# Optimization experiments

Hardware: AMD Instinct MI355X
Metric: run time of the kernel (lower is better)

The kernel has to match this reference:

```python
import jax, jax.numpy as jnp
import numpy as np


def setup_inputs() -> dict:
    key = jax.random.key(0)
    k1, k2, k3, k4, k5 = jax.random.split(key, 5)
    C, H, W, hi, wi = 32, 32, 32, 32, 32
    return {
        "lx_in": jax.random.normal(k1, (C, H, W, hi, wi), dtype=jnp.float32),
        "ux_in": jax.random.normal(k2, (C, H, W, hi, wi), dtype=jnp.float32),
        "lc_in": jax.random.normal(k3, (C, H, W), dtype=jnp.float32),
        "uc_in": jax.random.normal(k4, (C, H, W), dtype=jnp.float32),
        "x_min": jax.random.uniform(k5, (hi, wi), dtype=jnp.float32),
        "x_max": jnp.ones((hi, wi), dtype=jnp.float32),
    }


def reference(lx_in, ux_in, lc_in, uc_in, x_min, x_max):
    # lx_in/ux_in: [C,H,W,hi,wi] linear coeffs over input pixels; lc_in/uc_in: [C,H,W]
    minm = x_min[None, None, None, :, :]  # broadcast of x_min.repeat(C,H,W,1,1)
    maxm = x_max[None, None, None, :, :]
    zero = jnp.zeros((), lx_in.dtype)
    # lower concrete bound: positive coeff -> x_min, negative -> x_max (sign==0 -> 0 mask)
    mask_lower = jnp.where(lx_in > 0, minm, jnp.where(lx_in < 0, maxm, zero))
    l = jnp.sum(mask_lower * lx_in, axis=(-2, -1)) + lc_in  # [C,H,W]
    # upper concrete bound: positive coeff -> x_max, negative -> x_min
    mask_upper = jnp.where(ux_in > 0, maxm, jnp.where(ux_in < 0, minm, zero))
    u = jnp.sum(mask_upper * ux_in, axis=(-2, -1)) + uc_in  # [C,H,W]

    alive = l >= 0                      # pass-through branch (applied after dead branch in torch)
    cross = (l < 0) & (u > 0)           # crossing ReLU branch
    denom = jnp.where(cross, u - l, jnp.ones((), l.dtype))  # safe division
    slope = jnp.clip(jnp.where(cross, u / denom, jnp.ones((), l.dtype)), 0.0, 1.0)

    a5 = alive[..., None, None]
    c5 = cross[..., None, None]
    s5 = slope[..., None, None]
    lx_out = jnp.where(a5, lx_in, zero)
    ux_out = jnp.where(a5, ux_in, jnp.where(c5, s5 * ux_in, zero))
    lc_out = jnp.where(alive, lc_in, zero)
    uc_out = jnp.where(alive, uc_in, jnp.where(cross, slope * uc_in - slope * l, zero))
    return (lx_out, ux_out, lc_out, uc_out)
```

## Files before the change

### kernel.cpp

```cpp
#include <hip/hip_runtime.h>

constexpr int NPIX  = 32 * 32 * 32;
constexpr int TILE  = 32 * 32;
constexpr int NBIG  = NPIX * TILE;
constexpr int THREADS = 256;

__global__ __launch_bounds__(THREADS)
void relu_conv_kernel(const float* __restrict__ lx_in,
                      const float* __restrict__ ux_in,
                      const float* __restrict__ lc_in,
                      const float* __restrict__ uc_in,
                      const float* __restrict__ x_min,
                      const float* __restrict__ x_max,
                      float* __restrict__ lx_out,
                      float* __restrict__ ux_out,
                      float* __restrict__ lc_out,
                      float* __restrict__ uc_out)
{
    const int p = blockIdx.x;
    const int t = threadIdx.x;
    const long base = (long)p * TILE + t * 4;

    const float4 lx = *(const float4*)(lx_in + base);
    const float4 ux = *(const float4*)(ux_in + base);
    const float4 mn = *(const float4*)(x_min + t * 4);
    const float4 mx = *(const float4*)(x_max + t * 4);

    float sl = 0.f, su = 0.f;
    {
        const float a[4]  = {lx.x, lx.y, lx.z, lx.w};
        const float b[4]  = {ux.x, ux.y, ux.z, ux.w};
        const float lo[4] = {mn.x, mn.y, mn.z, mn.w};
        const float hi[4] = {mx.x, mx.y, mx.z, mx.w};
        #pragma unroll
        for (int i = 0; i < 4; ++i) {
            const float ml = a[i] > 0.f ? lo[i] : (a[i] < 0.f ? hi[i] : 0.f);
            const float mu = b[i] > 0.f ? hi[i] : (b[i] < 0.f ? lo[i] : 0.f);
            sl += ml * a[i];
            su += mu * b[i];
        }
    }

    #pragma unroll
    for (int off = 32; off > 0; off >>= 1) {
        sl += __shfl_down(sl, off, 64);
        su += __shfl_down(su, off, 64);
    }

    __shared__ float rl[4], ru[4];
    const int wave = t >> 6;
    if ((t & 63) == 0) { rl[wave] = sl; ru[wave] = su; }
    __syncthreads();

    const float lc = lc_in[p];
    const float uc = uc_in[p];
    const float l = (rl[0] + rl[1]) + (rl[2] + rl[3]) + lc;
    const float u = (ru[0] + ru[1]) + (ru[2] + ru[3]) + uc;

    const bool alive = (l >= 0.f);
    const bool cross = (l < 0.f) && (u > 0.f);
    float slope = cross ? (u / (u - l)) : 1.f;
    slope = fminf(fmaxf(slope, 0.f), 1.f);

    const float fl = alive ? 1.f : 0.f;
    const float fu = alive ? 1.f : (cross ? slope : 0.f);

    float4 lo4, uo4;
    lo4.x = fl * lx.x; lo4.y = fl * lx.y; lo4.z = fl * lx.z; lo4.w = fl * lx.w;
    uo4.x = fu * ux.x; uo4.y = fu * ux.y; uo4.z = fu * ux.z; uo4.w = fu * ux.w;

    *(float4*)(lx_out + base) = lo4;
    *(float4*)(ux_out + base) = uo4;

    if (t == 0) {
        lc_out[p] = alive ? lc : 0.f;
        uc_out[p] = alive ? uc : (cross ? (slope * uc - slope * l) : 0.f);
    }
}

extern "C" void kernel_launch(void* const* d_in, const int* in_sizes, int n_in,
                              void* d_out, int out_size, void* d_ws, size_t ws_size,
                              hipStream_t stream) {
    const float* lx_in = (const float*)d_in[0];
    const float* ux_in = (const float*)d_in[1];
    const float* lc_in = (const float*)d_in[2];
    const float* uc_in = (const float*)d_in[3];
    const float* x_min = (const float*)d_in[4];
    const float* x_max = (const float*)d_in[5];

    float* out = (float*)d_out;
    float* lx_out = out;
    float* ux_out = out + (size_t)NBIG;
    float* lc_out = out + (size_t)2 * NBIG;
    float* uc_out = lc_out + NPIX;

    relu_conv_kernel<<<dim3(NPIX), dim3(THREADS), 0, stream>>>(
        lx_in, ux_in, lc_in, uc_in, x_min, x_max,
        lx_out, ux_out, lc_out, uc_out);
}
```

Measured before the change: 436.3 us.

## Map one wave per pixel and use nontemporal vector loads and stores

```diff
diff --git a/kernel.cpp b/kernel.cpp
--- a/kernel.cpp
+++ b/kernel.cpp
@@ -2,8 +2,11 @@
 
 constexpr int NPIX  = 32 * 32 * 32;
 constexpr int TILE  = 32 * 32;
-constexpr int NBIG  = NPIX * TILE;
+constexpr long NBIG = (long)NPIX * TILE;
 constexpr int THREADS = 256;
+constexpr int PIX_PER_BLOCK = THREADS / 64;
+
+typedef float v4f __attribute__((ext_vector_type(4)));
 
 __global__ __launch_bounds__(THREADS)
 void relu_conv_kernel(const float* __restrict__ lx_in,
@@ -17,45 +20,45 @@
                       float* __restrict__ lc_out,
                       float* __restrict__ uc_out)
 {
-    const int p = blockIdx.x;
-    const int t = threadIdx.x;
-    const long base = (long)p * TILE + t * 4;
+    const int lane = threadIdx.x & 63;
+    const int wave = threadIdx.x >> 6;
+    const int p = blockIdx.x * PIX_PER_BLOCK + wave;
 
-    const float4 lx = *(const float4*)(lx_in + base);
-    const float4 ux = *(const float4*)(ux_in + base);
-    const float4 mn = *(const float4*)(x_min + t * 4);
-    const float4 mx = *(const float4*)(x_max + t * 4);
+    const long base = (long)p * TILE;
 
+    v4f lx[4], ux[4];
     float sl = 0.f, su = 0.f;
-    {
-        const float a[4]  = {lx.x, lx.y, lx.z, lx.w};
-        const float b[4]  = {ux.x, ux.y, ux.z, ux.w};
-        const float lo[4] = {mn.x, mn.y, mn.z, mn.w};
-        const float hi[4] = {mx.x, mx.y, mx.z, mx.w};
+    #pragma unroll
+    for (int j = 0; j < 4; ++j) {
+        const int off = lane * 4 + j * 256;
+        lx[j] = __builtin_nontemporal_load(
+                    reinterpret_cast<const v4f*>(lx_in + base + off));
+        ux[j] = __builtin_nontemporal_load(
+                    reinterpret_cast<const v4f*>(ux_in + base + off));
+        const v4f mn = *reinterpret_cast<const v4f*>(x_min + off);
+        const v4f mx = *reinterpret_cast<const v4f*>(x_max + off);
+
         #pragma unroll
-        for (int i = 0; i < 4; ++i) {
-            const float ml = a[i] > 0.f ? lo[i] : (a[i] < 0.f ? hi[i] : 0.f);
-            const float mu = b[i] > 0.f ? hi[i] : (b[i] < 0.f ? lo[i] : 0.f);
-            sl += ml * a[i];
-            su += mu * b[i];
+        for (int k = 0; k < 4; ++k) {
+            const float a = lx[j][k];
+            const float b = ux[j][k];
+            const float ml = a > 0.f ? mn[k] : (a < 0.f ? mx[k] : 0.f);
+            const float mu = b > 0.f ? mx[k] : (b < 0.f ? mn[k] : 0.f);
+            sl += ml * a;
+            su += mu * b;
         }
     }
 
     #pragma unroll
-    for (int off = 32; off > 0; off >>= 1) {
-        sl += __shfl_down(sl, off, 64);
-        su += __shfl_down(su, off, 64);
+    for (int m = 32; m > 0; m >>= 1) {
+        sl += __shfl_xor(sl, m, 64);
+        su += __shfl_xor(su, m, 64);
     }
-
-    __shared__ float rl[4], ru[4];
-    const int wave = t >> 6;
-    if ((t & 63) == 0) { rl[wave] = sl; ru[wave] = su; }
-    __syncthreads();
 
     const float lc = lc_in[p];
     const float uc = uc_in[p];
-    const float l = (rl[0] + rl[1]) + (rl[2] + rl[3]) + lc;
-    const float u = (ru[0] + ru[1]) + (ru[2] + ru[3]) + uc;
+    const float l = sl + lc;
+    const float u = su + uc;
 
     const bool alive = (l >= 0.f);
     const bool cross = (l < 0.f) && (u > 0.f);
@@ -65,14 +68,18 @@
     const float fl = alive ? 1.f : 0.f;
     const float fu = alive ? 1.f : (cross ? slope : 0.f);
 
-    float4 lo4, uo4;
-    lo4.x = fl * lx.x; lo4.y = fl * lx.y; lo4.z = fl * lx.z; lo4.w = fl * lx.w;
-    uo4.x = fu * ux.x; uo4.y = fu * ux.y; uo4.z = fu * ux.z; uo4.w = fu * ux.w;
+    #pragma unroll
+    for (int j = 0; j < 4; ++j) {
+        const int off = lane * 4 + j * 256;
+        v4f lo4 = lx[j] * fl;
+        v4f uo4 = ux[j] * fu;
+        __builtin_nontemporal_store(lo4,
+            reinterpret_cast<v4f*>(lx_out + base + off));
+        __builtin_nontemporal_store(uo4,
+            reinterpret_cast<v4f*>(ux_out + base + off));
+    }
 
-    *(float4*)(lx_out + base) = lo4;
-    *(float4*)(ux_out + base) = uo4;
-
-    if (t == 0) {
+    if (lane == 0) {
         lc_out[p] = alive ? lc : 0.f;
         uc_out[p] = alive ? uc : (cross ? (slope * uc - slope * l) : 0.f);
     }
@@ -90,11 +97,11 @@
 
     float* out = (float*)d_out;
     float* lx_out = out;
-    float* ux_out = out + (size_t)NBIG;
-    float* lc_out = out + (size_t)2 * NBIG;
+    float* ux_out = out + NBIG;
+    float* lc_out = out + 2 * NBIG;
     float* uc_out = lc_out + NPIX;
 
-    relu_conv_kernel<<<dim3(NPIX), dim3(THREADS), 0, stream>>>(
+    relu_conv_kernel<<<dim3(NPIX / PIX_PER_BLOCK), dim3(THREADS), 0, stream>>>(
         lx_in, ux_in, lc_in, uc_in, x_min, x_max,
         lx_out, ux_out, lc_out, uc_out);
 }
```

Result: faster. 424.0 us (-2.8%).
